# Performance work log

Hardware: AMD Instinct MI355X
Metric: run time of the kernel (lower is better)

The kernel has to match this reference:

```python
import jax, jax.numpy as jnp
import numpy as np

N_NODES = 50000
HEADS = 4
NEG_SLOPE = 0.2


def gat_layer(x, src, dst, W, a_src, a_dst, bias, num_nodes, heads):
    # x: [N, F_in]; W: [F_in, H*C]; a_src/a_dst: [H, C]; bias: [H*C]
    C = W.shape[1] // heads
    h = (x @ W).reshape(num_nodes, heads, C)               # [N, H, C]
    alpha_src = jnp.einsum('nhc,hc->nh', h, a_src)          # [N, H]
    alpha_dst = jnp.einsum('nhc,hc->nh', h, a_dst)          # [N, H]
    e = alpha_src[src] + alpha_dst[dst]                     # [E, H]
    e = jax.nn.leaky_relu(e, negative_slope=NEG_SLOPE)
    # edge-softmax over incoming edges of each destination node
    e_max = jax.ops.segment_max(e, dst, num_segments=num_nodes)  # [N, H]
    e = jnp.exp(e - e_max[dst])
    denom = jax.ops.segment_sum(e, dst, num_segments=num_nodes)  # [N, H]
    alpha = e / denom[dst]                                   # [E, H]
    msg = alpha[:, :, None] * h[src]                          # [E, H, C]
    out = jax.ops.segment_sum(msg, dst, num_segments=num_nodes)  # [N, H, C]
    return out.reshape(num_nodes, heads * C) + bias


def setup_inputs() -> dict:
    key = jax.random.key(0)
    ks = jax.random.split(key, 12)
    in_dim, hidden, out_dim, H = 128, 128, 128, HEADS
    c1, c2 = hidden // H, out_dim // H
    x = jax.random.normal(ks[0], (N_NODES, in_dim), dtype=jnp.float32)
    edge_index = jax.random.randint(ks[1], (2, 800000), 0, N_NODES, dtype=jnp.int64)
    g = lambda k, shp, fan: jax.random.normal(k, shp, dtype=jnp.float32) / np.sqrt(fan)
    return {
        'x': x,
        'edge_index': edge_index,
        'W1': g(ks[2], (in_dim, hidden), in_dim),
        'a_src1': g(ks[3], (H, c1), c1),
        'a_dst1': g(ks[4], (H, c1), c1),
        'b1': jnp.zeros((hidden,), jnp.float32),
        'W2': g(ks[5], (hidden, out_dim), hidden),
        'a_src2': g(ks[6], (H, c2), c2),
        'a_dst2': g(ks[7], (H, c2), c2),
        'b2': jnp.zeros((out_dim,), jnp.float32),
    }


def reference(x, edge_index, W1, a_src1, a_dst1, b1, W2, a_src2, a_dst2, b2):
    n = x.shape[0]
    # PyG GATConv default: add self-loops
    loops = jnp.arange(n, dtype=edge_index.dtype)
    src = jnp.concatenate([edge_index[0], loops])
    dst = jnp.concatenate([edge_index[1], loops])
    h = gat_layer(x, src, dst, W1, a_src1, a_dst1, b1, n, HEADS)
    h = jax.nn.relu(h)
    h = gat_layer(h, src, dst, W2, a_src2, a_dst2, b2, n, HEADS)
    return jax.nn.relu(h)
```

## Files before the change

### kernel.cpp

```cpp
#include <hip/hip_runtime.h>
#include <hip/hip_fp16.h>

#define HEADS 4
#define FEAT 128
#define NEG_SLOPE 0.2f
#define NPB 32
#define KT 32
#define SCAN_B 1024


__global__ void count_kernel(const int* __restrict__ dst, int* __restrict__ deg, int E) {
    int i = blockIdx.x * blockDim.x + threadIdx.x;
    int stride = gridDim.x * blockDim.x;
    for (; i < E; i += stride) atomicAdd(&deg[dst[i]], 1);
}

__global__ __launch_bounds__(SCAN_B) void scan_local_kernel(
        const int* __restrict__ deg, int* __restrict__ scanout,
        int* __restrict__ blocksums, int n) {
    __shared__ int tile[SCAN_B];
    int t = threadIdx.x;
    int i = blockIdx.x * SCAN_B + t;
    int v = (i < n) ? deg[i] : 0;
    tile[t] = v;
    __syncthreads();
    for (int off = 1; off < SCAN_B; off <<= 1) {
        int u = (t >= off) ? tile[t - off] : 0;
        __syncthreads();
        tile[t] += u;
        __syncthreads();
    }
    if (i < n) scanout[i] = tile[t];
    if (t == SCAN_B - 1) blocksums[blockIdx.x] = tile[SCAN_B - 1];
}

__global__ __launch_bounds__(SCAN_B) void scan_sums_kernel(int* __restrict__ blocksums, int nb) {
    __shared__ int tile[SCAN_B];
    int t = threadIdx.x;
    int v = (t < nb) ? blocksums[t] : 0;
    tile[t] = v;
    __syncthreads();
    for (int off = 1; off < SCAN_B; off <<= 1) {
        int u = (t >= off) ? tile[t - off] : 0;
        __syncthreads();
        tile[t] += u;
        __syncthreads();
    }
    int ex = (t == 0) ? 0 : tile[t - 1];
    if (t < nb) blocksums[t] = ex;
}

__global__ void scan_add_kernel(const int* __restrict__ scanout,
                                const int* __restrict__ blocksums,
                                int* __restrict__ offsets, int n) {
    int i = blockIdx.x * blockDim.x + threadIdx.x;
    if (i < n) offsets[i + 1] = scanout[i] + blocksums[i >> 10];
    if (i == 0) offsets[0] = 0;
}

__global__ void scatter_kernel(const int* __restrict__ src, const int* __restrict__ dst,
                               int* __restrict__ cursor, int* __restrict__ col, int E) {
    int i = blockIdx.x * blockDim.x + threadIdx.x;
    int stride = gridDim.x * blockDim.x;
    for (; i < E; i += stride) {
        int pos = atomicAdd(&cursor[dst[i]], 1);
        col[pos] = src[i];
    }
}


__global__ __launch_bounds__(256) void gemm_alpha_kernel(
        const float* __restrict__ x, const float* __restrict__ W,
        const float* __restrict__ a_src, const float* __restrict__ a_dst,
        __half* __restrict__ h, float* __restrict__ asrc_n,
        float* __restrict__ adst_n, int n_nodes) {
    __shared__ float xs[NPB][KT + 4];
    __shared__ float Ws[KT][FEAT];

    int t = threadIdx.x;
    int fgrp = t & 31;
    int f0 = fgrp * 4;
    int ngrp = t >> 5;
    int n0 = blockIdx.x * NPB;

    float acc[4][4];
    #pragma unroll
    for (int i = 0; i < 4; ++i)
        #pragma unroll
        for (int j = 0; j < 4; ++j) acc[i][j] = 0.f;

    for (int kt = 0; kt < FEAT; kt += KT) {
        {
            int node = t >> 3, q = t & 7;
            float4 v = make_float4(0.f, 0.f, 0.f, 0.f);
            if (n0 + node < n_nodes)
                v = *(const float4*)&x[(size_t)(n0 + node) * FEAT + kt + q * 4];
            *(float4*)&xs[node][q * 4] = v;
        }
        #pragma unroll
        for (int r = 0; r < 4; ++r) {
            int idx = t + r * 256;
            int row = idx >> 5, col4 = idx & 31;
            *(float4*)&Ws[row][col4 * 4] =
                *(const float4*)&W[(size_t)(kt + row) * FEAT + col4 * 4];
        }
        __syncthreads();

        #pragma unroll
        for (int kk = 0; kk < KT; kk += 4) {
            float4 w0 = *(const float4*)&Ws[kk + 0][f0];
            float4 w1 = *(const float4*)&Ws[kk + 1][f0];
            float4 w2 = *(const float4*)&Ws[kk + 2][f0];
            float4 w3 = *(const float4*)&Ws[kk + 3][f0];
            #pragma unroll
            for (int i = 0; i < 4; ++i) {
                float4 xv = *(const float4*)&xs[ngrp * 4 + i][kk];
                acc[i][0] += xv.x * w0.x + xv.y * w1.x + xv.z * w2.x + xv.w * w3.x;
                acc[i][1] += xv.x * w0.y + xv.y * w1.y + xv.z * w2.y + xv.w * w3.y;
                acc[i][2] += xv.x * w0.z + xv.y * w1.z + xv.z * w2.z + xv.w * w3.z;
                acc[i][3] += xv.x * w0.w + xv.y * w1.w + xv.z * w2.w + xv.w * w3.w;
            }
        }
        __syncthreads();
    }

    float4 as4 = *(const float4*)&a_src[f0];
    float4 ad4 = *(const float4*)&a_dst[f0];
    int head = fgrp >> 3;

    #pragma unroll
    for (int i = 0; i < 4; ++i) {
        int n = n0 + ngrp * 4 + i;
        bool ok = (n < n_nodes);
        if (ok) {
            __half2 ha = __floats2half2_rn(acc[i][0], acc[i][1]);
            __half2 hb = __floats2half2_rn(acc[i][2], acc[i][3]);
            *(__half2*)&h[n * FEAT + f0] = ha;
            *(__half2*)&h[n * FEAT + f0 + 2] = hb;
        }

        float ps = acc[i][0] * as4.x + acc[i][1] * as4.y + acc[i][2] * as4.z + acc[i][3] * as4.w;
        float pd = acc[i][0] * ad4.x + acc[i][1] * ad4.y + acc[i][2] * ad4.z + acc[i][3] * ad4.w;
        #pragma unroll
        for (int m = 4; m >= 1; m >>= 1) {
            ps += __shfl_xor(ps, m, 64);
            pd += __shfl_xor(pd, m, 64);
        }
        if (ok && (t & 7) == 0) {
            asrc_n[n * HEADS + head] = ps;
            adst_n[n * HEADS + head] = pd;
        }
    }
}


__global__ __launch_bounds__(256) void aggregate_kernel(
        const __half* __restrict__ h, const int* __restrict__ offsets,
        const int* __restrict__ col, const float* __restrict__ asrc_n,
        const float* __restrict__ adst_n, const float* __restrict__ bias,
        float* __restrict__ out, int n_nodes) {
    int wave = threadIdx.x >> 6;
    int lane = threadIdx.x & 63;
    int n = blockIdx.x * 4 + wave;
    if (n >= n_nodes) return;

    int head = lane >> 4;
    int lane2 = 2 * lane;
    int beg = offsets[n];
    int end = offsets[n + 1];
    float ad = adst_n[n * HEADS + head];

    float e_self = asrc_n[n * HEADS + head] + ad;
    e_self = e_self > 0.f ? e_self : NEG_SLOPE * e_self;
    float p = __expf(fminf(e_self, 60.f));
    float l = p;
    float2 hv = __half22float2(*(const __half2*)&h[n * FEAT + lane2]);
    float2 acc = make_float2(p * hv.x, p * hv.y);

    int j = beg;
    for (; j + 7 < end; j += 8) {
        int s[8];
        #pragma unroll
        for (int q = 0; q < 8; ++q) s[q] = col[j + q];
        float a[8];
        #pragma unroll
        for (int q = 0; q < 8; ++q) a[q] = asrc_n[s[q] * HEADS + head];
        __half2 hr[8];
        #pragma unroll
        for (int q = 0; q < 8; ++q) hr[q] = *(const __half2*)&h[s[q] * FEAT + lane2];
        #pragma unroll
        for (int q = 0; q < 8; ++q) {
            float e = a[q] + ad;
            e = e > 0.f ? e : NEG_SLOPE * e;
            float pe = __expf(fminf(e, 60.f));
            float2 hf = __half22float2(hr[q]);
            l += pe;
            acc.x += pe * hf.x;
            acc.y += pe * hf.y;
        }
    }
    for (; j + 3 < end; j += 4) {
        int s[4];
        #pragma unroll
        for (int q = 0; q < 4; ++q) s[q] = col[j + q];
        float a[4];
        #pragma unroll
        for (int q = 0; q < 4; ++q) a[q] = asrc_n[s[q] * HEADS + head];
        __half2 hr[4];
        #pragma unroll
        for (int q = 0; q < 4; ++q) hr[q] = *(const __half2*)&h[s[q] * FEAT + lane2];
        #pragma unroll
        for (int q = 0; q < 4; ++q) {
            float e = a[q] + ad;
            e = e > 0.f ? e : NEG_SLOPE * e;
            float pe = __expf(fminf(e, 60.f));
            float2 hf = __half22float2(hr[q]);
            l += pe;
            acc.x += pe * hf.x;
            acc.y += pe * hf.y;
        }
    }
    for (; j < end; ++j) {
        int s = col[j];
        float a = asrc_n[s * HEADS + head];
        float2 hs = __half22float2(*(const __half2*)&h[s * FEAT + lane2]);
        float e = a + ad;
        e = e > 0.f ? e : NEG_SLOPE * e;
        float pe = __expf(fminf(e, 60.f));
        l += pe;
        acc.x += pe * hs.x;
        acc.y += pe * hs.y;
    }

    float inv = 1.f / l;
    float2 bv = *(const float2*)&bias[lane2];
    float ox = acc.x * inv + bv.x;
    float oy = acc.y * inv + bv.y;
    float2 o = make_float2(ox > 0.f ? ox : 0.f, oy > 0.f ? oy : 0.f);
    *(float2*)&out[n * FEAT + lane2] = o;
}


static inline size_t align_up(size_t v, size_t a) { return (v + a - 1) & ~(a - 1); }

extern "C" void kernel_launch(void* const* d_in, const int* in_sizes, int n_in,
                              void* d_out, int out_size, void* d_ws, size_t ws_size,
                              hipStream_t stream) {
    const float* x   = (const float*)d_in[0];
    const int*   ei  = (const int*)d_in[1];
    const float* W1  = (const float*)d_in[2];
    const float* as1 = (const float*)d_in[3];
    const float* ad1 = (const float*)d_in[4];
    const float* b1  = (const float*)d_in[5];
    const float* W2  = (const float*)d_in[6];
    const float* as2 = (const float*)d_in[7];
    const float* ad2 = (const float*)d_in[8];
    const float* b2  = (const float*)d_in[9];

    int N = in_sizes[0] / FEAT;
    int E = in_sizes[1] / 2;
    const int* src_idx = ei;
    const int* dst_idx = ei + E;

    int nsb = (N + SCAN_B - 1) / SCAN_B;

    char* p = (char*)d_ws;
    auto alloc = [&](size_t bytes) {
        char* r = p;
        p += align_up(bytes, 256);
        return r;
    };
    int*    deg      = (int*)alloc((size_t)N * 4);
    int*    offsets  = (int*)alloc((size_t)(N + 1) * 4);
    int*    cursor   = (int*)alloc((size_t)N * 4);
    int*    col      = (int*)alloc((size_t)E * 4);
    int*    scanout  = (int*)alloc((size_t)N * 4);
    int*    blocksum = (int*)alloc((size_t)nsb * 4);
    __half* h        = (__half*)alloc((size_t)N * FEAT * 2);
    float*  asn      = (float*)alloc((size_t)N * HEADS * 4);
    float*  adn      = (float*)alloc((size_t)N * HEADS * 4);
    float*  buf1     = (float*)d_out;

    hipMemsetAsync(deg, 0, (size_t)N * 4, stream);
    count_kernel<<<1024, 256, 0, stream>>>(dst_idx, deg, E);
    scan_local_kernel<<<nsb, SCAN_B, 0, stream>>>(deg, scanout, blocksum, N);
    scan_sums_kernel<<<1, SCAN_B, 0, stream>>>(blocksum, nsb);
    scan_add_kernel<<<(N + 255) / 256, 256, 0, stream>>>(scanout, blocksum, offsets, N);
    hipMemcpyAsync(cursor, offsets, (size_t)N * 4, hipMemcpyDeviceToDevice, stream);
    scatter_kernel<<<1024, 256, 0, stream>>>(src_idx, dst_idx, cursor, col, E);

    int gemm_grid = (N + NPB - 1) / NPB;
    int agg_grid = (N + 3) / 4;

    gemm_alpha_kernel<<<gemm_grid, 256, 0, stream>>>(x, W1, as1, ad1, h, asn, adn, N);
    aggregate_kernel<<<agg_grid, 256, 0, stream>>>(h, offsets, col, asn, adn, b1, buf1, N);

    gemm_alpha_kernel<<<gemm_grid, 256, 0, stream>>>(buf1, W2, as2, ad2, h, asn, adn, N);
    aggregate_kernel<<<agg_grid, 256, 0, stream>>>(h, offsets, col, asn, adn, b2, (float*)d_out, N);
}
```

Baseline: 354.8 us.

## Use fp16 MFMA for node feature GEMM with pre-transposed half weights

```diff
diff --git a/kernel.cpp b/kernel.cpp
--- a/kernel.cpp
+++ b/kernel.cpp
@@ -4,9 +4,12 @@
 #define HEADS 4
 #define FEAT 128
 #define NEG_SLOPE 0.2f
-#define NPB 32
-#define KT 32
 #define SCAN_B 1024
+#define GPAD 136
+
+typedef _Float16 half8 __attribute__((ext_vector_type(8)));
+typedef _Float16 half4v __attribute__((ext_vector_type(4)));
+typedef float f32x4 __attribute__((ext_vector_type(4)));
 
 
 __global__ void count_kernel(const int* __restrict__ dst, int* __restrict__ deg, int E) {
@@ -69,86 +72,97 @@
 }
 
 
+__global__ void wtrans_kernel(const float* __restrict__ W, __half* __restrict__ wt) {
+    int t = threadIdx.x;
+    #pragma unroll
+    for (int i = 0; i < 8; ++i) {
+        int flat = blockIdx.x * 2048 + i * 256 + t;
+        int k = flat >> 7, f = flat & 127;
+        wt[f * 128 + k] = __float2half(W[k * 128 + f]);
+    }
+}
+
+
 __global__ __launch_bounds__(256) void gemm_alpha_kernel(
-        const float* __restrict__ x, const float* __restrict__ W,
+        const float* __restrict__ x, const __half* __restrict__ wt,
         const float* __restrict__ a_src, const float* __restrict__ a_dst,
         __half* __restrict__ h, float* __restrict__ asrc_n,
         float* __restrict__ adst_n, int n_nodes) {
-    __shared__ float xs[NPB][KT + 4];
-    __shared__ float Ws[KT][FEAT];
+    __shared__ _Float16 xs[64 * GPAD];
+    __shared__ _Float16 ws[128 * GPAD];
 
     int t = threadIdx.x;
-    int fgrp = t & 31;
-    int f0 = fgrp * 4;
-    int ngrp = t >> 5;
-    int n0 = blockIdx.x * NPB;
-
-    float acc[4][4];
-    #pragma unroll
-    for (int i = 0; i < 4; ++i)
-        #pragma unroll
-        for (int j = 0; j < 4; ++j) acc[i][j] = 0.f;
-
-    for (int kt = 0; kt < FEAT; kt += KT) {
-        {
-            int node = t >> 3, q = t & 7;
-            float4 v = make_float4(0.f, 0.f, 0.f, 0.f);
-            if (n0 + node < n_nodes)
-                v = *(const float4*)&x[(size_t)(n0 + node) * FEAT + kt + q * 4];
-            *(float4*)&xs[node][q * 4] = v;
-        }
-        #pragma unroll
-        for (int r = 0; r < 4; ++r) {
-            int idx = t + r * 256;
-            int row = idx >> 5, col4 = idx & 31;
-            *(float4*)&Ws[row][col4 * 4] =
-                *(const float4*)&W[(size_t)(kt + row) * FEAT + col4 * 4];
-        }
-        __syncthreads();
-
-        #pragma unroll
-        for (int kk = 0; kk < KT; kk += 4) {
-            float4 w0 = *(const float4*)&Ws[kk + 0][f0];
-            float4 w1 = *(const float4*)&Ws[kk + 1][f0];
-            float4 w2 = *(const float4*)&Ws[kk + 2][f0];
-            float4 w3 = *(const float4*)&Ws[kk + 3][f0];
+    int n0 = blockIdx.x * 64;
+
+    #pragma unroll
+    for (int i = 0; i < 8; ++i) {
+        int flat = t + i * 256;
+        int row = flat >> 5, q = flat & 31;
+        float4 v = make_float4(0.f, 0.f, 0.f, 0.f);
+        if (n0 + row < n_nodes) v = *(const float4*)&x[(n0 + row) * FEAT + q * 4];
+        half4v hv = { (_Float16)v.x, (_Float16)v.y, (_Float16)v.z, (_Float16)v.w };
+        *(half4v*)&xs[row * GPAD + q * 4] = hv;
+    }
+    #pragma unroll
+    for (int i = 0; i < 8; ++i) {
+        int flat = t + i * 256;
+        int row = flat >> 4, c = flat & 15;
+        half8 v = *(const half8*)&wt[row * 128 + c * 8];
+        *(half8*)&ws[row * GPAD + c * 8] = v;
+    }
+    __syncthreads();
+
+    int wv = t >> 6, l = t & 63;
+    int lr = l & 15, lk = (l >> 4) * 8;
+
+    f32x4 acc[8];
+    #pragma unroll
+    for (int i = 0; i < 8; ++i) acc[i] = (f32x4){0.f, 0.f, 0.f, 0.f};
+
+    const _Float16* xrow = &xs[(wv * 16 + lr) * GPAD + lk];
+    #pragma unroll
+    for (int ks = 0; ks < 4; ++ks) {
+        half8 a = *(const half8*)&xrow[ks * 32];
+        #pragma unroll
+        for (int f8 = 0; f8 < 8; ++f8) {
+            half8 b = *(const half8*)&ws[(f8 * 16 + lr) * GPAD + ks * 32 + lk];
+            acc[f8] = __builtin_amdgcn_mfma_f32_16x16x32_f16(a, b, acc[f8], 0, 0, 0);
+        }
+    }
+
+    float asv[8], adv[8];
+    #pragma unroll
+    for (int f8 = 0; f8 < 8; ++f8) {
+        asv[f8] = a_src[f8 * 16 + lr];
+        adv[f8] = a_dst[f8 * 16 + lr];
+    }
+    #pragma unroll
+    for (int r = 0; r < 4; ++r) {
+        int n = n0 + wv * 16 + (l >> 4) * 4 + r;
+        bool ok = (n < n_nodes);
+        float ps[4] = {0.f, 0.f, 0.f, 0.f};
+        float pd[4] = {0.f, 0.f, 0.f, 0.f};
+        #pragma unroll
+        for (int f8 = 0; f8 < 8; ++f8) {
+            float v = acc[f8][r];
+            if (ok) h[n * FEAT + f8 * 16 + lr] = __float2half(v);
+            ps[f8 >> 1] += v * asv[f8];
+            pd[f8 >> 1] += v * adv[f8];
+        }
+        #pragma unroll
+        for (int m = 1; m <= 8; m <<= 1) {
             #pragma unroll
-            for (int i = 0; i < 4; ++i) {
-                float4 xv = *(const float4*)&xs[ngrp * 4 + i][kk];
-                acc[i][0] += xv.x * w0.x + xv.y * w1.x + xv.z * w2.x + xv.w * w3.x;
-                acc[i][1] += xv.x * w0.y + xv.y * w1.y + xv.z * w2.y + xv.w * w3.y;
-                acc[i][2] += xv.x * w0.z + xv.y * w1.z + xv.z * w2.z + xv.w * w3.z;
-                acc[i][3] += xv.x * w0.w + xv.y * w1.w + xv.z * w2.w + xv.w * w3.w;
+            for (int hd = 0; hd < 4; ++hd) {
+                ps[hd] += __shfl_xor(ps[hd], m, 64);
+                pd[hd] += __shfl_xor(pd[hd], m, 64);
             }
         }
-        __syncthreads();
-    }
-
-    float4 as4 = *(const float4*)&a_src[f0];
-    float4 ad4 = *(const float4*)&a_dst[f0];
-    int head = fgrp >> 3;
-
-    #pragma unroll
-    for (int i = 0; i < 4; ++i) {
-        int n = n0 + ngrp * 4 + i;
-        bool ok = (n < n_nodes);
-        if (ok) {
-            __half2 ha = __floats2half2_rn(acc[i][0], acc[i][1]);
-            __half2 hb = __floats2half2_rn(acc[i][2], acc[i][3]);
-            *(__half2*)&h[n * FEAT + f0] = ha;
-            *(__half2*)&h[n * FEAT + f0 + 2] = hb;
-        }
-
-        float ps = acc[i][0] * as4.x + acc[i][1] * as4.y + acc[i][2] * as4.z + acc[i][3] * as4.w;
-        float pd = acc[i][0] * ad4.x + acc[i][1] * ad4.y + acc[i][2] * ad4.z + acc[i][3] * ad4.w;
-        #pragma unroll
-        for (int m = 4; m >= 1; m >>= 1) {
-            ps += __shfl_xor(ps, m, 64);
-            pd += __shfl_xor(pd, m, 64);
-        }
-        if (ok && (t & 7) == 0) {
-            asrc_n[n * HEADS + head] = ps;
-            adst_n[n * HEADS + head] = pd;
+        if (ok && lr == 0) {
+            #pragma unroll
+            for (int hd = 0; hd < 4; ++hd) {
+                asrc_n[n * HEADS + hd] = ps[hd];
+                adst_n[n * HEADS + hd] = pd[hd];
+            }
         }
     }
 }
@@ -277,24 +291,28 @@
     int*    scanout  = (int*)alloc((size_t)N * 4);
     int*    blocksum = (int*)alloc((size_t)nsb * 4);
     __half* h        = (__half*)alloc((size_t)N * FEAT * 2);
+    __half* wt1      = (__half*)alloc((size_t)FEAT * FEAT * 2);
+    __half* wt2      = (__half*)alloc((size_t)FEAT * FEAT * 2);
     float*  asn      = (float*)alloc((size_t)N * HEADS * 4);
     float*  adn      = (float*)alloc((size_t)N * HEADS * 4);
     float*  buf1     = (float*)d_out;
 
     hipMemsetAsync(deg, 0, (size_t)N * 4, stream);
     count_kernel<<<1024, 256, 0, stream>>>(dst_idx, deg, E);
+    wtrans_kernel<<<8, 256, 0, stream>>>(W1, wt1);
+    wtrans_kernel<<<8, 256, 0, stream>>>(W2, wt2);
     scan_local_kernel<<<nsb, SCAN_B, 0, stream>>>(deg, scanout, blocksum, N);
     scan_sums_kernel<<<1, SCAN_B, 0, stream>>>(blocksum, nsb);
     scan_add_kernel<<<(N + 255) / 256, 256, 0, stream>>>(scanout, blocksum, offsets, N);
     hipMemcpyAsync(cursor, offsets, (size_t)N * 4, hipMemcpyDeviceToDevice, stream);
     scatter_kernel<<<1024, 256, 0, stream>>>(src_idx, dst_idx, cursor, col, E);
 
-    int gemm_grid = (N + NPB - 1) / NPB;
+    int gemm_grid = (N + 63) / 64;
     int agg_grid = (N + 3) / 4;
 
-    gemm_alpha_kernel<<<gemm_grid, 256, 0, stream>>>(x, W1, as1, ad1, h, asn, adn, N);
+    gemm_alpha_kernel<<<gemm_grid, 256, 0, stream>>>(x, wt1, as1, ad1, h, asn, adn, N);
     aggregate_kernel<<<agg_grid, 256, 0, stream>>>(h, offsets, col, asn, adn, b1, buf1, N);
 
-    gemm_alpha_kernel<<<gemm_grid, 256, 0, stream>>>(buf1, W2, as2, ad2, h, asn, adn, N);
+    gemm_alpha_kernel<<<gemm_grid, 256, 0, stream>>>(buf1, wt2, as2, ad2, h, asn, adn, N);
     aggregate_kernel<<<agg_grid, 256, 0, stream>>>(h, offsets, col, asn, adn, b2, (float*)d_out, N);
 }
```

Result: faster. 317.1 us (-10.6%).
